# Optimization experiments

Measured on AMD Instinct MI355X. Metric: run time of the kernel, lower is better.

## Reference

```python
import jax, jax.numpy as jnp
import numpy as np
from jax import lax

N, C, H, W = 4, 64, 256, 256
S = 500  # samples per image per set
EPS = 1e-5

def _conv3x3(x, w, b):
    y = lax.conv_general_dilated(x, w, (1, 1), 'SAME', dimension_numbers=('NCHW', 'OIHW', 'NCHW'))
    return y + b[None, :, None, None]

def _bn2d(x, g, b):
    m = x.mean(axis=(0, 2, 3), keepdims=True)
    v = x.var(axis=(0, 2, 3), keepdims=True)
    return g[None, :, None, None] * (x - m) * lax.rsqrt(v + EPS) + b[None, :, None, None]

def _conv_block(x, w1, b1, g1, be1, w2, b2, g2, be2):
    x = jax.nn.relu(_bn2d(_conv3x3(x, w1, b1), g1, be1))
    x = jax.nn.relu(_bn2d(_conv3x3(x, w2, b2), g2, be2))
    return x

def setup_inputs():
    key = jax.random.key(0)
    ks = jax.random.split(key, 40)
    inp = {'x': jax.random.normal(ks[0], (N, C, H, W), jnp.float32)}
    inp['query_pos_sets'] = jax.random.uniform(ks[1], (N, 1, H, W)) < 0.1
    inp['query_neg_sets'] = jax.random.uniform(ks[2], (N, 1, H, W)) < 0.5
    for i, name in enumerate(['easy_pos_idx', 'easy_neg_idx', 'hard_pos_idx', 'hard_neg_idx']):
        inp[name] = jax.random.randint(ks[3 + i], (N, S), 0, N * H * W, jnp.int32)
    k = 7
    for pre in ['e', 'p']:
        for j in ['1', '2']:
            inp[pre + '_w' + j] = jax.random.normal(ks[k], (C, C, 3, 3), jnp.float32) * 0.05
            k += 1
            inp[pre + '_b' + j] = jnp.zeros((C,), jnp.float32)
            inp[pre + '_g' + j] = jnp.ones((C,), jnp.float32)
            inp[pre + '_be' + j] = jnp.zeros((C,), jnp.float32)
    inp['l_w'] = jax.random.normal(ks[k], (C, C), jnp.float32) * 0.05
    inp['l_b'] = jnp.zeros((C,), jnp.float32)
    inp['l_g'] = jnp.ones((C,), jnp.float32)
    inp['l_be'] = jnp.zeros((C,), jnp.float32)
    return inp

def reference(x, query_pos_sets, query_neg_sets, easy_pos_idx, easy_neg_idx, hard_pos_idx, hard_neg_idx,
              e_w1, e_b1, e_g1, e_be1, e_w2, e_b2, e_g2, e_be2,
              p_w1, p_b1, p_g1, p_be1, p_w2, p_b2, p_g2, p_be2,
              l_w, l_b, l_g, l_be):
    # encoder (num_convs=1 conv_block), projector conv_block, then linear_block
    x_enc = _conv_block(x, e_w1, e_b1, e_g1, e_be1, e_w2, e_b2, e_g2, e_be2)
    x_pro = _conv_block(x_enc, p_w1, p_b1, p_g1, p_be1, p_w2, p_b2, p_g2, p_be2)
    x_pro = x_pro.transpose(0, 2, 3, 1).reshape(-1, C)  # [N*H*W, C]
    y = x_pro @ l_w.T + l_b                              # Linear
    m = y.mean(axis=0, keepdims=True)                    # BatchNorm1d (train stats)
    v = y.var(axis=0, keepdims=True)
    y = jax.nn.relu(l_g * (y - m) * lax.rsqrt(v + EPS) + l_be)
    # keeps is all-True (see source comments) -> x_pro[keeps_all] == y
    feat = y.reshape(N, H, W, C)
    pos_m = query_pos_sets[:, 0].astype(y.dtype)         # [N,H,W]
    neg_m = query_neg_sets[:, 0].astype(y.dtype)
    query_pos = jnp.einsum('nhwc,nhw->nc', feat, pos_m) / pos_m.sum(axis=(1, 2))[:, None]
    query_neg = jnp.einsum('nhwc,nhw->nc', feat, neg_m) / neg_m.sum(axis=(1, 2))[:, None]
    sample_easy_pos = y[easy_pos_idx.reshape(-1)]        # [N*S, C]
    sample_easy_neg = y[easy_neg_idx.reshape(-1)]
    sample_hard_pos = y[hard_pos_idx.reshape(-1)]
    sample_hard_neg = y[hard_neg_idx.reshape(-1)]
    return (x_enc, query_pos[:, None, :], query_neg[:, None, :],
            sample_easy_pos, sample_easy_neg, sample_hard_pos, sample_hard_neg)
```

## Files before the change

### kernel.cpp

```cpp
#include <hip/hip_runtime.h>

#define HW 65536
#define CHW (64*HW)
#define NHW 262144
#define EPSV 1e-5f

typedef __attribute__((ext_vector_type(8))) short short8;
typedef __attribute__((ext_vector_type(4))) float f32x4;


__device__ inline void bn_params(const float* __restrict__ acc, int stage,
                                 const float* __restrict__ g, const float* __restrict__ be,
                                 int c, float& scale, float& shift) {
    const float invM = 1.f / 262144.f;
    float s  = acc[stage*128 + c];
    float ss = acc[stage*128 + 64 + c];
    float mean = s * invM;
    float var  = ss * invM - mean*mean;
    float sc = g[c] * rsqrtf(var + EPSV);
    scale = sc;
    shift = fmaf(-mean, sc, be[c]);
}

__device__ inline unsigned short f2bf(float f) {
    unsigned int u = __float_as_uint(f);
    return (unsigned short)((u + 0x7fffu + ((u >> 16) & 1u)) >> 16);
}
__device__ inline float bf2f(short u) {
    return __uint_as_float(((unsigned)(unsigned short)u) << 16);
}

__global__ __launch_bounds__(256) void k_wpack(const float* __restrict__ w, unsigned short* __restrict__ wpk) {
    int tid = blockIdx.x*256 + threadIdx.x;
    if (tid >= 36864) return;
    int fb = tid >> 9, rem = tid & 511, l = rem >> 3, j = rem & 7;
    int tap = fb >> 3, ks = (fb >> 2) & 1, cg = fb & 3;
    int ci = ks*32 + ((l >> 4) << 3) + j;
    int co = cg*16 + (l & 15);
    wpk[tid] = f2bf(w[co*576 + ci*9 + tap]);
}

template<bool CL_IN>
__global__ __launch_bounds__(256) void k_convmf(
    const void* __restrict__ in_, const unsigned short* __restrict__ wpk,
    unsigned short* __restrict__ outCL, const float* __restrict__ accb, int stage,
    const float* __restrict__ g, const float* __restrict__ be,
    float* __restrict__ statsacc, int out_stage)
{
    __shared__ unsigned short s_in[20736];
    __shared__ float s_scale[64], s_shift[64];
    __shared__ float sacc[128];
    const int t = threadIdx.x;
    const int tx = blockIdx.x, ty = blockIdx.y, n = blockIdx.z;
    if (stage >= 0 && t < 64) {
        float sc, sh; bn_params(accb, stage, g, be, t, sc, sh);
        s_scale[t] = sc; s_shift[t] = sh;
    }
    if (t < 128) sacc[t] = 0.f;
    __syncthreads();
    if (CL_IN) {
        const unsigned short* in = (const unsigned short*)in_;
#pragma unroll 1
        for (int i = t; i < 2592; i += 256) {
            int p = i >> 3, ck = i & 7;
            int py = p / 18, px = p - py*18;
            int gy = ty*16 + py - 1, gx = tx*16 + px - 1;
            short8 v;
            if ((unsigned)gy < 256u && (unsigned)gx < 256u) {
                v = *(const short8*)(in + ((((n << 16) + (gy << 8) + gx) << 6) + (ck << 3)));
                if (stage >= 0) {
#pragma unroll
                    for (int jj = 0; jj < 8; ++jj) {
                        int cc = (ck << 3) + jj;
                        float f = bf2f(v[jj]);
                        f = fmaxf(fmaf(f, s_scale[cc], s_shift[cc]), 0.f);
                        v[jj] = (short)f2bf(f);
                    }
                }
            } else {
#pragma unroll
                for (int jj = 0; jj < 8; ++jj) v[jj] = 0;
            }
            int byte = p*128 + (((ck << 4)) ^ ((p & 7) << 4));
            *(short8*)((char*)s_in + byte) = v;
        }
    } else {
        const float* in = (const float*)in_;
#pragma unroll 1
        for (int oct = 0; oct < 8; ++oct) {
#pragma unroll 1
            for (int p = t; p < 324; p += 256) {
                int py = p / 18, px = p - py*18;
                int gy = ty*16 + py - 1, gx = tx*16 + px - 1;
                short8 pk;
                if ((unsigned)gy < 256u && (unsigned)gx < 256u) {
                    const float* ip = in + (((n*64 + oct*8) << 16) + (gy << 8) + gx);
#pragma unroll
                    for (int jj = 0; jj < 8; ++jj) {
                        float v = ip[jj << 16];
                        if (stage >= 0) {
                            int cc = oct*8 + jj;
                            v = fmaxf(fmaf(v, s_scale[cc], s_shift[cc]), 0.f);
                        }
                        pk[jj] = (short)f2bf(v);
                    }
                } else {
#pragma unroll
                    for (int jj = 0; jj < 8; ++jj) pk[jj] = 0;
                }
                int byte = p*128 + ((oct*16) ^ ((p & 7) << 4));
                *(short8*)((char*)s_in + byte) = pk;
            }
        }
    }
    __syncthreads();
    const int wv = t >> 6, l = t & 63;
    const int lr = l & 15, lq = l >> 4;
    const int wv4 = wv * 4;
    f32x4 acc[4][4];
#pragma unroll
    for (int i = 0; i < 4; ++i)
#pragma unroll
        for (int jj = 0; jj < 4; ++jj)
            acc[i][jj] = (f32x4)0.f;

#pragma unroll
    for (int tap = 0; tap < 9; ++tap) {
        const int ty_off = tap / 3, tx_off = tap % 3;
#pragma unroll
        for (int ks = 0; ks < 2; ++ks) {
            short8 wf[4], pf[4];
#pragma unroll
            for (int cg = 0; cg < 4; ++cg)
                wf[cg] = *(const short8*)(wpk + (((tap*2 + ks)*4 + cg) << 9) + (l << 3));
#pragma unroll
            for (int row = 0; row < 4; ++row) {
                int p = (wv4 + row + ty_off)*18 + lr + tx_off;
                int byte = p*128 + ((lq*16 + ks*64) ^ ((p & 7) << 4));
                pf[row] = *(const short8*)((const char*)s_in + byte);
            }
#pragma unroll
            for (int row = 0; row < 4; ++row)
#pragma unroll
                for (int cg = 0; cg < 4; ++cg)
                    acc[row][cg] = __builtin_amdgcn_mfma_f32_16x16x32_bf16(
                        wf[cg], pf[row], acc[row][cg], 0, 0, 0);
        }
    }
    const int gx = tx*16 + lr;
#pragma unroll
    for (int row = 0; row < 4; ++row) {
        const int gy = ty*16 + wv4 + row;
        const int pix = (n << 16) + (gy << 8) + gx;
#pragma unroll
        for (int cg = 0; cg < 4; ++cg) {
            uint2 pk;
            pk.x = (unsigned)f2bf(acc[row][cg][0]) | ((unsigned)f2bf(acc[row][cg][1]) << 16);
            pk.y = (unsigned)f2bf(acc[row][cg][2]) | ((unsigned)f2bf(acc[row][cg][3]) << 16);
            *(uint2*)(outCL + ((pix << 6) + (cg << 4) + (lq << 2))) = pk;
        }
    }
    float s_l[4][4], ss_l[4][4];
#pragma unroll
    for (int cg = 0; cg < 4; ++cg)
#pragma unroll
        for (int r = 0; r < 4; ++r) { s_l[cg][r] = 0.f; ss_l[cg][r] = 0.f; }
#pragma unroll
    for (int row = 0; row < 4; ++row)
#pragma unroll
        for (int cg = 0; cg < 4; ++cg)
#pragma unroll
            for (int r = 0; r < 4; ++r) {
                float v = acc[row][cg][r];
                s_l[cg][r] += v;
                ss_l[cg][r] = fmaf(v, v, ss_l[cg][r]);
            }
#pragma unroll
    for (int k = 1; k <= 8; k <<= 1)
#pragma unroll
        for (int cg = 0; cg < 4; ++cg)
#pragma unroll
            for (int r = 0; r < 4; ++r) {
                s_l[cg][r]  += __shfl_xor(s_l[cg][r],  k);
                ss_l[cg][r] += __shfl_xor(ss_l[cg][r], k);
            }
    if (lr == 0) {
#pragma unroll
        for (int cg = 0; cg < 4; ++cg)
#pragma unroll
            for (int r = 0; r < 4; ++r) {
                int co = cg*16 + lq*4 + r;
                atomicAdd(&sacc[co], s_l[cg][r]);
                atomicAdd(&sacc[64 + co], ss_l[cg][r]);
            }
    }
    __syncthreads();
    if (t < 128) atomicAdd(&statsacc[out_stage*128 + t], sacc[t]);
}

__global__ __launch_bounds__(256) void k_apply(
    const unsigned short* __restrict__ inCL, float* __restrict__ out,
    const float* __restrict__ acc, int stage,
    const float* __restrict__ g, const float* __restrict__ be)
{
    __shared__ float s_v[64][257];
    __shared__ float s_scale[64], s_shift[64];
    const int t = threadIdx.x;
    const int n = blockIdx.x >> 8, gy = blockIdx.x & 255;
    if (t < 64) { float sc, sh; bn_params(acc, stage, g, be, t, sc, sh); s_scale[t] = sc; s_shift[t] = sh; }
    __syncthreads();
    const unsigned short* ip = inCL + ((((n << 8) + gy) << 8) + t)*64;
#pragma unroll
    for (int ck = 0; ck < 8; ++ck) {
        short8 v = *(const short8*)(ip + (ck << 3));
#pragma unroll
        for (int jj = 0; jj < 8; ++jj) {
            int c = (ck << 3) + jj;
            s_v[c][t] = fmaxf(fmaf(bf2f(v[jj]), s_scale[c], s_shift[c]), 0.f);
        }
    }
    __syncthreads();
#pragma unroll 1
    for (int i = t; i < 16384; i += 256) {
        int c = i >> 8, x = i & 255;
        out[((n*64 + c) << 16) + (gy << 8) + x] = s_v[c][x];
    }
}

__global__ __launch_bounds__(256) void k_linear(
    const unsigned short* __restrict__ inCL, const float* __restrict__ lw,
    float* __restrict__ y, const float* __restrict__ acc, int stage,
    const float* __restrict__ g, const float* __restrict__ be)
{
    __shared__ float s_x[64][257];
    __shared__ float s_scale[64], s_shift[64];
    const int t = threadIdx.x;
    const int nh = blockIdx.x;
    if (t < 64) { float sc, sh; bn_params(acc, stage, g, be, t, sc, sh); s_scale[t] = sc; s_shift[t] = sh; }
    __syncthreads();
    const unsigned short* ip = inCL + (((nh << 8) + t) << 6);
#pragma unroll
    for (int ck = 0; ck < 8; ++ck) {
        short8 v = *(const short8*)(ip + (ck << 3));
#pragma unroll
        for (int jj = 0; jj < 8; ++jj) {
            int c = (ck << 3) + jj;
            s_x[c][t] = fmaxf(fmaf(bf2f(v[jj]), s_scale[c], s_shift[c]), 0.f);
        }
    }
    __syncthreads();
    float a[64];
#pragma unroll
    for (int i = 0; i < 64; ++i) a[i] = 0.f;
#pragma unroll 1
    for (int ci = 0; ci < 64; ++ci) {
        float v = s_x[ci][t];
#pragma unroll
        for (int co = 0; co < 64; ++co) a[co] = fmaf(v, lw[(co << 6) + ci], a[co]);
    }
    float4* yp = (float4*)(y + (size_t)nh*16384 + t*64);
#pragma unroll
    for (int q = 0; q < 16; ++q)
        yp[q] = make_float4(a[4*q], a[4*q+1], a[4*q+2], a[4*q+3]);
}

__global__ __launch_bounds__(256) void k_stats1d(const float* __restrict__ y, float* __restrict__ acc) {
    __shared__ float l_s[4][64], l_ss[4][64];
    const int t = threadIdx.x;
    const int c = t & 63, rg = t >> 6;
    float s = 0.f, ss = 0.f;
    for (int e = blockIdx.x*256 + t; e < 16777216; e += 1024*256) {
        float v = y[e];
        s += v; ss = fmaf(v, v, ss);
    }
    l_s[rg][c] = s; l_ss[rg][c] = ss;
    __syncthreads();
    if (t < 64) {
        s  = l_s[0][t] + l_s[1][t] + l_s[2][t] + l_s[3][t];
        ss = l_ss[0][t] + l_ss[1][t] + l_ss[2][t] + l_ss[3][t];
        atomicAdd(&acc[512 + t], s);
        atomicAdd(&acc[512 + 64 + t], ss);
    }
}

__global__ __launch_bounds__(256) void k_queries(
    const float* __restrict__ y, const int* __restrict__ mpos, const int* __restrict__ mneg,
    float* __restrict__ acc, const float* __restrict__ g, const float* __restrict__ be)
{
    __shared__ float l_sp[4][64], l_sn[4][64];
    __shared__ float l_cp[4], l_cn[4];
    const int t = threadIdx.x;
    const int c = t & 63, rg = t >> 6;
    const int n = blockIdx.x >> 8, chunk = blockIdx.x & 255;
    float sc, sh; bn_params(acc, 4, g, be, c, sc, sh);
    float sp = 0.f, sn = 0.f, cp = 0.f, cn = 0.f;
    const int p0 = (n << 16) + (chunk << 8);
#pragma unroll 1
    for (int i = rg; i < 256; i += 4) {
        int p = p0 + i;
        float v = fmaxf(fmaf(y[p*64 + c], sc, sh), 0.f);
        float mp = (float)mpos[p], mn = (float)mneg[p];
        sp = fmaf(mp, v, sp); sn = fmaf(mn, v, sn);
        cp += mp; cn += mn;
    }
    l_sp[rg][c] = sp; l_sn[rg][c] = sn;
    if (c == 0) { l_cp[rg] = cp; l_cn[rg] = cn; }
    __syncthreads();
    if (t < 64) {
        atomicAdd(&acc[640 + (n << 6) + t], l_sp[0][t] + l_sp[1][t] + l_sp[2][t] + l_sp[3][t]);
        atomicAdd(&acc[896 + (n << 6) + t], l_sn[0][t] + l_sn[1][t] + l_sn[2][t] + l_sn[3][t]);
    } else if (t == 64) {
        atomicAdd(&acc[1152 + n], l_cp[0] + l_cp[1] + l_cp[2] + l_cp[3]);
        atomicAdd(&acc[1156 + n], l_cn[0] + l_cn[1] + l_cn[2] + l_cn[3]);
    }
}

__global__ __launch_bounds__(256) void k_gather(
    const float* __restrict__ y,
    const int* __restrict__ i0, const int* __restrict__ i1,
    const int* __restrict__ i2, const int* __restrict__ i3,
    const float* __restrict__ acc, const float* __restrict__ g, const float* __restrict__ be,
    float* __restrict__ out)
{
    const int gid = blockIdx.x*256 + threadIdx.x;
    const int c = gid & 63;
    const int j = gid >> 6;
    const int set = j / 2000, i = j - set*2000;
    const int* idx = (set == 0) ? i0 : (set == 1) ? i1 : (set == 2) ? i2 : i3;
    const int p = idx[i];
    float sc, sh; bn_params(acc, 4, g, be, c, sc, sh);
    out[16777728 + gid] = fmaxf(fmaf(y[p*64 + c], sc, sh), 0.f);
}

__global__ __launch_bounds__(256) void k_qwrite(const float* __restrict__ acc, float* __restrict__ out) {
    int j = blockIdx.x*256 + threadIdx.x;
    if (j < 512) {
        int which = j >> 8, nn = (j >> 6) & 3, cc = j & 63;
        out[16777216 + j] = acc[640 + (which << 8) + (nn << 6) + cc] / acc[1152 + (which << 2) + nn];
    }
}

extern "C" void kernel_launch(void* const* d_in, const int* in_sizes, int n_in,
                              void* d_out, int out_size, void* d_ws, size_t ws_size,
                              hipStream_t stream) {
    (void)in_sizes; (void)n_in; (void)out_size; (void)ws_size;
    const float* x     = (const float*)d_in[0];
    const int*   mpos  = (const int*)d_in[1];
    const int*   mneg  = (const int*)d_in[2];
    const int*   ep    = (const int*)d_in[3];
    const int*   en    = (const int*)d_in[4];
    const int*   hp    = (const int*)d_in[5];
    const int*   hn    = (const int*)d_in[6];
    const float* e_w1  = (const float*)d_in[7];
    const float* e_g1  = (const float*)d_in[9];
    const float* e_be1 = (const float*)d_in[10];
    const float* e_w2  = (const float*)d_in[11];
    const float* e_g2  = (const float*)d_in[13];
    const float* e_be2 = (const float*)d_in[14];
    const float* p_w1  = (const float*)d_in[15];
    const float* p_g1  = (const float*)d_in[17];
    const float* p_be1 = (const float*)d_in[18];
    const float* p_w2  = (const float*)d_in[19];
    const float* p_g2  = (const float*)d_in[21];
    const float* p_be2 = (const float*)d_in[22];
    const float* l_w   = (const float*)d_in[23];
    const float* l_g   = (const float*)d_in[25];
    const float* l_be  = (const float*)d_in[26];
    float* out = (float*)d_out;

    unsigned short* b0 = (unsigned short*)d_ws;
    unsigned short* b1 = b0 + 16777216;
    float* y   = (float*)(b1 + 16777216);
    float* acc = y + 16777216;
    unsigned short* wpk = (unsigned short*)(acc + 4096);

    hipMemsetAsync(acc, 0, 1280*sizeof(float), stream);
    k_wpack<<<144, 256, 0, stream>>>(e_w1, wpk);
    k_wpack<<<144, 256, 0, stream>>>(e_w2, wpk + 36864);
    k_wpack<<<144, 256, 0, stream>>>(p_w1, wpk + 2*36864);
    k_wpack<<<144, 256, 0, stream>>>(p_w2, wpk + 3*36864);

    dim3 cgrid(16, 16, 4);
    k_convmf<false><<<cgrid, 256, 0, stream>>>(x,  wpk,           b0, acc, -1, nullptr, nullptr, acc, 0);
    k_convmf<true ><<<cgrid, 256, 0, stream>>>(b0, wpk +   36864, b1, acc,  0, e_g1, e_be1, acc, 1);
    k_apply<<<1024, 256, 0, stream>>>(b1, out, acc, 1, e_g2, e_be2);
    k_convmf<true ><<<cgrid, 256, 0, stream>>>(b1, wpk + 2*36864, b0, acc,  1, e_g2, e_be2, acc, 2);
    k_convmf<true ><<<cgrid, 256, 0, stream>>>(b0, wpk + 3*36864, b1, acc,  2, p_g1, p_be1, acc, 3);
    k_linear<<<1024, 256, 0, stream>>>(b1, l_w, y, acc, 3, p_g2, p_be2);
    k_stats1d<<<1024, 256, 0, stream>>>(y, acc);
    k_queries<<<1024, 256, 0, stream>>>(y, mpos, mneg, acc, l_g, l_be);
    k_qwrite<<<2, 256, 0, stream>>>(acc, out);
    k_gather<<<2000, 256, 0, stream>>>(y, ep, en, hp, hn, acc, l_g, l_be, out);
}
```

Measured before the change: 568.4 us.

## Restructure conv pipeline: pre-transpose input, 512-thread conv, bf16 linear output with fused stats

Adds a transpose kernel that converts the fp32 NCHW input to bf16 channels-last, so every conv reads the same layout. The conv now runs 512 threads per block, with each wave computing half the output channels, and uses a remapped block order. The smem swizzle moves into the global read address so stores are linear. The linear layer now writes bf16 instead of fp32 and accumulates the BatchNorm1d statistics itself, which removes the separate stats pass and halves the traffic for later reads of y. The risk is lower precision in y and more atomic and shuffle work inside the linear kernel.

```diff
diff --git a/kernel.cpp b/kernel.cpp
--- a/kernel.cpp
+++ b/kernel.cpp
@@ -26,8 +26,8 @@
     unsigned int u = __float_as_uint(f);
     return (unsigned short)((u + 0x7fffu + ((u >> 16) & 1u)) >> 16);
 }
-__device__ inline float bf2f(short u) {
-    return __uint_as_float(((unsigned)(unsigned short)u) << 16);
+__device__ inline float bf2f(unsigned short u) {
+    return __uint_as_float(((unsigned)u) << 16);
 }
 
 __global__ __launch_bounds__(256) void k_wpack(const float* __restrict__ w, unsigned short* __restrict__ wpk) {
@@ -40,9 +40,26 @@
     wpk[tid] = f2bf(w[co*576 + ci*9 + tap]);
 }
 
-template<bool CL_IN>
-__global__ __launch_bounds__(256) void k_convmf(
-    const void* __restrict__ in_, const unsigned short* __restrict__ wpk,
+__global__ __launch_bounds__(256) void k_xpose(const float* __restrict__ x, unsigned short* __restrict__ xcl) {
+    __shared__ unsigned short s_b[64][257];
+    const int t = threadIdx.x;
+    const int n = blockIdx.x >> 8, gy = blockIdx.x & 255;
+    const float* ip = x + ((n << 6) << 16) + (gy << 8) + t;
+#pragma unroll
+    for (int c = 0; c < 64; ++c) s_b[c][t] = f2bf(ip[c << 16]);
+    __syncthreads();
+    unsigned short* op = xcl + (size_t)((((n << 8) + gy) << 8) + t) * 64;
+#pragma unroll
+    for (int ck = 0; ck < 8; ++ck) {
+        short8 v;
+#pragma unroll
+        for (int jj = 0; jj < 8; ++jj) v[jj] = (short)s_b[ck*8 + jj][t];
+        *(short8*)(op + (ck << 3)) = v;
+    }
+}
+
+__global__ __launch_bounds__(512) void k_convmf(
+    const unsigned short* __restrict__ in, const unsigned short* __restrict__ wpk,
     unsigned short* __restrict__ outCL, const float* __restrict__ accb, int stage,
     const float* __restrict__ g, const float* __restrict__ be,
     float* __restrict__ statsacc, int out_stage)
@@ -51,77 +68,48 @@
     __shared__ float s_scale[64], s_shift[64];
     __shared__ float sacc[128];
     const int t = threadIdx.x;
-    const int tx = blockIdx.x, ty = blockIdx.y, n = blockIdx.z;
+    const int id = blockIdx.x;
+    const int sid = (id & 7)*128 + (id >> 3);
+    const int tx = sid & 15, ty = (sid >> 4) & 15, n = sid >> 8;
     if (stage >= 0 && t < 64) {
         float sc, sh; bn_params(accb, stage, g, be, t, sc, sh);
         s_scale[t] = sc; s_shift[t] = sh;
     }
     if (t < 128) sacc[t] = 0.f;
     __syncthreads();
-    if (CL_IN) {
-        const unsigned short* in = (const unsigned short*)in_;
-#pragma unroll 1
-        for (int i = t; i < 2592; i += 256) {
-            int p = i >> 3, ck = i & 7;
-            int py = p / 18, px = p - py*18;
-            int gy = ty*16 + py - 1, gx = tx*16 + px - 1;
-            short8 v;
-            if ((unsigned)gy < 256u && (unsigned)gx < 256u) {
-                v = *(const short8*)(in + ((((n << 16) + (gy << 8) + gx) << 6) + (ck << 3)));
-                if (stage >= 0) {
-#pragma unroll
-                    for (int jj = 0; jj < 8; ++jj) {
-                        int cc = (ck << 3) + jj;
-                        float f = bf2f(v[jj]);
-                        f = fmaxf(fmaf(f, s_scale[cc], s_shift[cc]), 0.f);
-                        v[jj] = (short)f2bf(f);
-                    }
+#pragma unroll 1
+    for (int i = t; i < 2592; i += 512) {
+        int p = i >> 3, ck = i & 7;
+        int py = p / 18, px = p - py*18;
+        int gy = ty*16 + py - 1, gx = tx*16 + px - 1;
+        short8 v;
+        if ((unsigned)gy < 256u && (unsigned)gx < 256u) {
+            int cksrc = ck ^ (p & 7);
+            v = *(const short8*)(in + ((size_t)((n << 16) + (gy << 8) + gx) << 6) + (cksrc << 3));
+            if (stage >= 0) {
+#pragma unroll
+                for (int jj = 0; jj < 8; ++jj) {
+                    int cc = (cksrc << 3) + jj;
+                    float f = bf2f((unsigned short)v[jj]);
+                    f = fmaxf(fmaf(f, s_scale[cc], s_shift[cc]), 0.f);
+                    v[jj] = (short)f2bf(f);
                 }
-            } else {
-#pragma unroll
-                for (int jj = 0; jj < 8; ++jj) v[jj] = 0;
-            }
-            int byte = p*128 + (((ck << 4)) ^ ((p & 7) << 4));
-            *(short8*)((char*)s_in + byte) = v;
-        }
-    } else {
-        const float* in = (const float*)in_;
-#pragma unroll 1
-        for (int oct = 0; oct < 8; ++oct) {
-#pragma unroll 1
-            for (int p = t; p < 324; p += 256) {
-                int py = p / 18, px = p - py*18;
-                int gy = ty*16 + py - 1, gx = tx*16 + px - 1;
-                short8 pk;
-                if ((unsigned)gy < 256u && (unsigned)gx < 256u) {
-                    const float* ip = in + (((n*64 + oct*8) << 16) + (gy << 8) + gx);
-#pragma unroll
-                    for (int jj = 0; jj < 8; ++jj) {
-                        float v = ip[jj << 16];
-                        if (stage >= 0) {
-                            int cc = oct*8 + jj;
-                            v = fmaxf(fmaf(v, s_scale[cc], s_shift[cc]), 0.f);
-                        }
-                        pk[jj] = (short)f2bf(v);
-                    }
-                } else {
-#pragma unroll
-                    for (int jj = 0; jj < 8; ++jj) pk[jj] = 0;
-                }
-                int byte = p*128 + ((oct*16) ^ ((p & 7) << 4));
-                *(short8*)((char*)s_in + byte) = pk;
-            }
-        }
+            }
+        } else {
+#pragma unroll
+            for (int jj = 0; jj < 8; ++jj) v[jj] = 0;
+        }
+        *(short8*)((char*)s_in + p*128 + (ck << 4)) = v;
     }
     __syncthreads();
     const int wv = t >> 6, l = t & 63;
     const int lr = l & 15, lq = l >> 4;
-    const int wv4 = wv * 4;
-    f32x4 acc[4][4];
+    const int wr = wv & 3, wc = wv >> 2;
+    f32x4 acc[4][2];
 #pragma unroll
     for (int i = 0; i < 4; ++i)
 #pragma unroll
-        for (int jj = 0; jj < 4; ++jj)
+        for (int jj = 0; jj < 2; ++jj)
             acc[i][jj] = (f32x4)0.f;
 
 #pragma unroll
@@ -129,69 +117,70 @@
         const int ty_off = tap / 3, tx_off = tap % 3;
 #pragma unroll
         for (int ks = 0; ks < 2; ++ks) {
-            short8 wf[4], pf[4];
-#pragma unroll
-            for (int cg = 0; cg < 4; ++cg)
-                wf[cg] = *(const short8*)(wpk + (((tap*2 + ks)*4 + cg) << 9) + (l << 3));
+            short8 wf[2], pf[4];
+#pragma unroll
+            for (int cgi = 0; cgi < 2; ++cgi)
+                wf[cgi] = *(const short8*)(wpk + (((tap*2 + ks)*4 + wc*2 + cgi) << 9) + (l << 3));
 #pragma unroll
             for (int row = 0; row < 4; ++row) {
-                int p = (wv4 + row + ty_off)*18 + lr + tx_off;
+                int p = (wr*4 + row + ty_off)*18 + lr + tx_off;
                 int byte = p*128 + ((lq*16 + ks*64) ^ ((p & 7) << 4));
                 pf[row] = *(const short8*)((const char*)s_in + byte);
             }
 #pragma unroll
             for (int row = 0; row < 4; ++row)
 #pragma unroll
-                for (int cg = 0; cg < 4; ++cg)
-                    acc[row][cg] = __builtin_amdgcn_mfma_f32_16x16x32_bf16(
-                        wf[cg], pf[row], acc[row][cg], 0, 0, 0);
+                for (int cgi = 0; cgi < 2; ++cgi)
+                    acc[row][cgi] = __builtin_amdgcn_mfma_f32_16x16x32_bf16(
+                        wf[cgi], pf[row], acc[row][cgi], 0, 0, 0);
         }
     }
     const int gx = tx*16 + lr;
 #pragma unroll
     for (int row = 0; row < 4; ++row) {
-        const int gy = ty*16 + wv4 + row;
-        const int pix = (n << 16) + (gy << 8) + gx;
-#pragma unroll
-        for (int cg = 0; cg < 4; ++cg) {
+        const int gy = ty*16 + wr*4 + row;
+        const size_t pix = (size_t)((n << 16) + (gy << 8) + gx);
+#pragma unroll
+        for (int cgi = 0; cgi < 2; ++cgi) {
+            const int cgg = wc*2 + cgi;
             uint2 pk;
-            pk.x = (unsigned)f2bf(acc[row][cg][0]) | ((unsigned)f2bf(acc[row][cg][1]) << 16);
-            pk.y = (unsigned)f2bf(acc[row][cg][2]) | ((unsigned)f2bf(acc[row][cg][3]) << 16);
-            *(uint2*)(outCL + ((pix << 6) + (cg << 4) + (lq << 2))) = pk;
-        }
-    }
-    float s_l[4][4], ss_l[4][4];
-#pragma unroll
-    for (int cg = 0; cg < 4; ++cg)
-#pragma unroll
-        for (int r = 0; r < 4; ++r) { s_l[cg][r] = 0.f; ss_l[cg][r] = 0.f; }
+            pk.x = (unsigned)f2bf(acc[row][cgi][0]) | ((unsigned)f2bf(acc[row][cgi][1]) << 16);
+            pk.y = (unsigned)f2bf(acc[row][cgi][2]) | ((unsigned)f2bf(acc[row][cgi][3]) << 16);
+            *(uint2*)(outCL + ((pix << 6) + (cgg << 4) + (lq << 2))) = pk;
+        }
+    }
+    float s_l[2][4], ss_l[2][4];
+#pragma unroll
+    for (int cgi = 0; cgi < 2; ++cgi)
+#pragma unroll
+        for (int r = 0; r < 4; ++r) { s_l[cgi][r] = 0.f; ss_l[cgi][r] = 0.f; }
 #pragma unroll
     for (int row = 0; row < 4; ++row)
 #pragma unroll
-        for (int cg = 0; cg < 4; ++cg)
+        for (int cgi = 0; cgi < 2; ++cgi)
 #pragma unroll
             for (int r = 0; r < 4; ++r) {
-                float v = acc[row][cg][r];
-                s_l[cg][r] += v;
-                ss_l[cg][r] = fmaf(v, v, ss_l[cg][r]);
+                float v = acc[row][cgi][r];
+                s_l[cgi][r] += v;
+                ss_l[cgi][r] = fmaf(v, v, ss_l[cgi][r]);
             }
 #pragma unroll
     for (int k = 1; k <= 8; k <<= 1)
 #pragma unroll
-        for (int cg = 0; cg < 4; ++cg)
+        for (int cgi = 0; cgi < 2; ++cgi)
 #pragma unroll
             for (int r = 0; r < 4; ++r) {
-                s_l[cg][r]  += __shfl_xor(s_l[cg][r],  k);
-                ss_l[cg][r] += __shfl_xor(ss_l[cg][r], k);
+                s_l[cgi][r]  += __shfl_xor(s_l[cgi][r],  k);
+                ss_l[cgi][r] += __shfl_xor(ss_l[cgi][r], k);
             }
     if (lr == 0) {
 #pragma unroll
-        for (int cg = 0; cg < 4; ++cg)
+        for (int cgi = 0; cgi < 2; ++cgi)
 #pragma unroll
             for (int r = 0; r < 4; ++r) {
-                int co = cg*16 + lq*4 + r;
-                atomicAdd(&sacc[co], s_l[cg][r]);
-                atomicAdd(&sacc[64 + co], ss_l[cg][r]);
+                int co = (wc*2 + cgi)*16 + lq*4 + r;
+                atomicAdd(&sacc[co], s_l[cgi][r]);
+                atomicAdd(&sacc[64 + co], ss_l[cgi][r]);
             }
     }
     __syncthreads();
@@ -209,14 +198,14 @@
     const int n = blockIdx.x >> 8, gy = blockIdx.x & 255;
     if (t < 64) { float sc, sh; bn_params(acc, stage, g, be, t, sc, sh); s_scale[t] = sc; s_shift[t] = sh; }
     __syncthreads();
-    const unsigned short* ip = inCL + ((((n << 8) + gy) << 8) + t)*64;
+    const unsigned short* ip = inCL + (size_t)((((n << 8) + gy) << 8) + t)*64;
 #pragma unroll
     for (int ck = 0; ck < 8; ++ck) {
         short8 v = *(const short8*)(ip + (ck << 3));
 #pragma unroll
         for (int jj = 0; jj < 8; ++jj) {
             int c = (ck << 3) + jj;
-            s_v[c][t] = fmaxf(fmaf(bf2f(v[jj]), s_scale[c], s_shift[c]), 0.f);
+            s_v[c][t] = fmaxf(fmaf(bf2f((unsigned short)v[jj]), s_scale[c], s_shift[c]), 0.f);
         }
     }
     __syncthreads();
@@ -229,23 +218,25 @@
 
 __global__ __launch_bounds__(256) void k_linear(
     const unsigned short* __restrict__ inCL, const float* __restrict__ lw,
-    float* __restrict__ y, const float* __restrict__ acc, int stage,
+    unsigned short* __restrict__ y, float* __restrict__ acc, int stage,
     const float* __restrict__ g, const float* __restrict__ be)
 {
     __shared__ float s_x[64][257];
     __shared__ float s_scale[64], s_shift[64];
+    __shared__ float sacc2[128];
     const int t = threadIdx.x;
     const int nh = blockIdx.x;
     if (t < 64) { float sc, sh; bn_params(acc, stage, g, be, t, sc, sh); s_scale[t] = sc; s_shift[t] = sh; }
-    __syncthreads();
-    const unsigned short* ip = inCL + (((nh << 8) + t) << 6);
+    if (t < 128) sacc2[t] = 0.f;
+    __syncthreads();
+    const unsigned short* ip = inCL + ((size_t)((nh << 8) + t) << 6);
 #pragma unroll
     for (int ck = 0; ck < 8; ++ck) {
         short8 v = *(const short8*)(ip + (ck << 3));
 #pragma unroll
         for (int jj = 0; jj < 8; ++jj) {
             int c = (ck << 3) + jj;
-            s_x[c][t] = fmaxf(fmaf(bf2f(v[jj]), s_scale[c], s_shift[c]), 0.f);
+            s_x[c][t] = fmaxf(fmaf(bf2f((unsigned short)v[jj]), s_scale[c], s_shift[c]), 0.f);
         }
     }
     __syncthreads();
@@ -258,33 +249,31 @@
 #pragma unroll
         for (int co = 0; co < 64; ++co) a[co] = fmaf(v, lw[(co << 6) + ci], a[co]);
     }
-    float4* yp = (float4*)(y + (size_t)nh*16384 + t*64);
-#pragma unroll
-    for (int q = 0; q < 16; ++q)
-        yp[q] = make_float4(a[4*q], a[4*q+1], a[4*q+2], a[4*q+3]);
-}
-
-__global__ __launch_bounds__(256) void k_stats1d(const float* __restrict__ y, float* __restrict__ acc) {
-    __shared__ float l_s[4][64], l_ss[4][64];
-    const int t = threadIdx.x;
-    const int c = t & 63, rg = t >> 6;
-    float s = 0.f, ss = 0.f;
-    for (int e = blockIdx.x*256 + t; e < 16777216; e += 1024*256) {
-        float v = y[e];
-        s += v; ss = fmaf(v, v, ss);
-    }
-    l_s[rg][c] = s; l_ss[rg][c] = ss;
-    __syncthreads();
-    if (t < 64) {
-        s  = l_s[0][t] + l_s[1][t] + l_s[2][t] + l_s[3][t];
-        ss = l_ss[0][t] + l_ss[1][t] + l_ss[2][t] + l_ss[3][t];
-        atomicAdd(&acc[512 + t], s);
-        atomicAdd(&acc[512 + 64 + t], ss);
-    }
+    unsigned short* yp = y + ((size_t)nh*256 + t)*64;
+#pragma unroll
+    for (int ck = 0; ck < 8; ++ck) {
+        short8 v;
+#pragma unroll
+        for (int jj = 0; jj < 8; ++jj) v[jj] = (short)f2bf(a[ck*8 + jj]);
+        *(short8*)(yp + (ck << 3)) = v;
+    }
+    const int l = t & 63;
+    float mys = 0.f, myss = 0.f;
+#pragma unroll 1
+    for (int co = 0; co < 64; ++co) {
+        float s = a[co], q = a[co]*a[co];
+#pragma unroll
+        for (int k = 1; k <= 32; k <<= 1) { s += __shfl_xor(s, k); q += __shfl_xor(q, k); }
+        if (l == co) { mys = s; myss = q; }
+    }
+    atomicAdd(&sacc2[l], mys);
+    atomicAdd(&sacc2[64 + l], myss);
+    __syncthreads();
+    if (t < 128) atomicAdd(&acc[512 + t], sacc2[t]);
 }
 
 __global__ __launch_bounds__(256) void k_queries(
-    const float* __restrict__ y, const int* __restrict__ mpos, const int* __restrict__ mneg,
+    const unsigned short* __restrict__ y, const int* __restrict__ mpos, const int* __restrict__ mneg,
     float* __restrict__ acc, const float* __restrict__ g, const float* __restrict__ be)
 {
     __shared__ float l_sp[4][64], l_sn[4][64];
@@ -298,7 +287,7 @@
 #pragma unroll 1
     for (int i = rg; i < 256; i += 4) {
         int p = p0 + i;
-        float v = fmaxf(fmaf(y[p*64 + c], sc, sh), 0.f);
+        float v = fmaxf(fmaf(bf2f(y[(size_t)p*64 + c]), sc, sh), 0.f);
         float mp = (float)mpos[p], mn = (float)mneg[p];
         sp = fmaf(mp, v, sp); sn = fmaf(mn, v, sn);
         cp += mp; cn += mn;
@@ -316,7 +305,7 @@
 }
 
 __global__ __launch_bounds__(256) void k_gather(
-    const float* __restrict__ y,
+    const unsigned short* __restrict__ y,
     const int* __restrict__ i0, const int* __restrict__ i1,
     const int* __restrict__ i2, const int* __restrict__ i3,
     const float* __restrict__ acc, const float* __restrict__ g, const float* __restrict__ be,
@@ -329,7 +318,7 @@
     const int* idx = (set == 0) ? i0 : (set == 1) ? i1 : (set == 2) ? i2 : i3;
     const int p = idx[i];
     float sc, sh; bn_params(acc, 4, g, be, c, sc, sh);
-    out[16777728 + gid] = fmaxf(fmaf(y[p*64 + c], sc, sh), 0.f);
+    out[16777728 + gid] = fmaxf(fmaf(bf2f(y[(size_t)p*64 + c]), sc, sh), 0.f);
 }
 
 __global__ __launch_bounds__(256) void k_qwrite(const float* __restrict__ acc, float* __restrict__ out) {
@@ -368,10 +357,11 @@
     const float* l_be  = (const float*)d_in[26];
     float* out = (float*)d_out;
 
-    unsigned short* b0 = (unsigned short*)d_ws;
+    unsigned short* bx = (unsigned short*)d_ws;
+    unsigned short* b0 = bx + 16777216;
     unsigned short* b1 = b0 + 16777216;
-    float* y   = (float*)(b1 + 16777216);
-    float* acc = y + 16777216;
+    unsigned short* yb = b1 + 16777216;
+    float* acc = (float*)(yb + 16777216);
     unsigned short* wpk = (unsigned short*)(acc + 4096);
 
     hipMemsetAsync(acc, 0, 1280*sizeof(float), stream);
@@ -379,16 +369,15 @@
     k_wpack<<<144, 256, 0, stream>>>(e_w2, wpk + 36864);
     k_wpack<<<144, 256, 0, stream>>>(p_w1, wpk + 2*36864);
     k_wpack<<<144, 256, 0, stream>>>(p_w2, wpk + 3*36864);
-
-    dim3 cgrid(16, 16, 4);
-    k_convmf<false><<<cgrid, 256, 0, stream>>>(x,  wpk,           b0, acc, -1, nullptr, nullptr, acc, 0);
-    k_convmf<true ><<<cgrid, 256, 0, stream>>>(b0, wpk +   36864, b1, acc,  0, e_g1, e_be1, acc, 1);
+    k_xpose<<<1024, 256, 0, stream>>>(x, bx);
+
+    k_convmf<<<1024, 512, 0, stream>>>(bx, wpk,           b0, acc, -1, nullptr, nullptr, acc, 0);
+    k_convmf<<<1024, 512, 0, stream>>>(b0, wpk +   36864, b1, acc,  0, e_g1, e_be1, acc, 1);
     k_apply<<<1024, 256, 0, stream>>>(b1, out, acc, 1, e_g2, e_be2);
-    k_convmf<true ><<<cgrid, 256, 0, stream>>>(b1, wpk + 2*36864, b0, acc,  1, e_g2, e_be2, acc, 2);
-    k_convmf<true ><<<cgrid, 256, 0, stream>>>(b0, wpk + 3*36864, b1, acc,  2, p_g1, p_be1, acc, 3);
-    k_linear<<<1024, 256, 0, stream>>>(b1, l_w, y, acc, 3, p_g2, p_be2);
-    k_stats1d<<<1024, 256, 0, stream>>>(y, acc);
-    k_queries<<<1024, 256, 0, stream>>>(y, mpos, mneg, acc, l_g, l_be);
+    k_convmf<<<1024, 512, 0, stream>>>(b1, wpk + 2*36864, b0, acc,  1, e_g2, e_be2, acc, 2);
+    k_convmf<<<1024, 512, 0, stream>>>(b0, wpk + 3*36864, b1, acc,  2, p_g1, p_be1, acc, 3);
+    k_linear<<<1024, 256, 0, stream>>>(b1, l_w, yb, acc, 3, p_g2, p_be2);
+    k_queries<<<1024, 256, 0, stream>>>(yb, mpos, mneg, acc, l_g, l_be);
     k_qwrite<<<2, 256, 0, stream>>>(acc, out);
-    k_gather<<<2000, 256, 0, stream>>>(y, ep, en, hp, hn, acc, l_g, l_be, out);
-}
+    k_gather<<<2000, 256, 0, stream>>>(yb, ep, en, hp, hn, acc, l_g, l_be, out);
+}
```

Result: no change. 568.1 us (-0.0%).
